# Optimization experiments

Measured on AMD Instinct MI355X. Metric: run time of the kernel, lower is better.

## Reference

```python
import jax, jax.numpy as jnp
import numpy as np

B, NPG, H = 128, 111, 32
N = B * NPG                 # 14208 total nodes
EPG = NPG * (NPG - 1)       # 12210 directed edges per connectome graph
E = B * EPG                 # 1562880 edges total


def setup_inputs() -> dict:
    key = jax.random.key(0)
    # full directed graph (no self loops) within each of the B graphs
    s, d = np.nonzero(~np.eye(NPG, dtype=bool))
    off = (np.arange(B) * NPG)[:, None]
    edge_index = jnp.asarray(
        np.stack([(s[None] + off).ravel(), (d[None] + off).ravel()]),
        dtype=jnp.int32)
    ks = iter(jax.random.split(key, 32))
    def nrm(shape, scale=0.1):
        return (jax.random.normal(next(ks), shape) * scale).astype(jnp.float32)
    inp = {
        'x': nrm((N, 1), 1.0),
        'edge_index': edge_index,
        'edge_attr': nrm((E, 2), 1.0),
    }
    dims = [1, H, H]  # input dim of each GATConv layer
    for l in range(3):
        inp[f'W{l}'] = nrm((dims[l], H))   # lin weight (no bias in PyG lin)
        inp[f'as{l}'] = nrm((H,))          # att_src
        inp[f'ad{l}'] = nrm((H,))          # att_dst
        inp[f'We{l}'] = nrm((2, H))        # lin_edge weight
        inp[f'ae{l}'] = nrm((H,))          # att_edge
        inp[f'b{l}'] = jnp.zeros((H,), jnp.float32)
    inp['lin_W'] = nrm((H, 1))
    inp['lin_b'] = jnp.zeros((1,), jnp.float32)
    return inp


def _gat(x, src, dst, ea, W, a_s, a_d, We, a_e, b):
    """PyG GATConv, heads=1: edge-feature attention + segment softmax over dst."""
    h = x @ W                                                     # [N,H]
    alpha = (h @ a_s)[src] + (h @ a_d)[dst] + (ea @ We) @ a_e     # [E']
    alpha = jax.nn.leaky_relu(alpha, 0.2)
    m = jax.lax.stop_gradient(jax.ops.segment_max(alpha, dst, num_segments=N))
    ex = jnp.exp(alpha - m[dst])
    coef = ex / jax.ops.segment_sum(ex, dst, num_segments=N)[dst]
    return jax.ops.segment_sum(coef[:, None] * h[src], dst, num_segments=N) + b


def reference(x, edge_index, edge_attr,
              W0, as0, ad0, We0, ae0, b0,
              W1, as1, ad1, We1, ae1, b1,
              W2, as2, ad2, We2, ae2, b2,
              lin_W, lin_b):
    src0, dst0 = edge_index[0], edge_index[1]
    # add_self_loops with fill_value='mean': per-dst mean of incoming edge_attr
    deg = jax.ops.segment_sum(jnp.ones((E,), edge_attr.dtype), dst0, num_segments=N)
    ea_loop = jax.ops.segment_sum(edge_attr, dst0, num_segments=N) / jnp.maximum(deg, 1.0)[:, None]
    loop = jnp.arange(N, dtype=src0.dtype)
    src = jnp.concatenate([src0, loop])
    dst = jnp.concatenate([dst0, loop])
    ea = jnp.concatenate([edge_attr, ea_loop], axis=0)

    h = _gat(x, src, dst, ea, W0, as0, ad0, We0, ae0, b0)
    h = _gat(h, src, dst, ea, W1, as1, ad1, We1, ae1, b1)
    h = jax.nn.relu(h)  # Dropout(0.5) is identity in eval
    h = _gat(h, src, dst, ea, W2, as2, ad2, We2, ae2, b2)

    graph_id = jnp.arange(N) // NPG                                # global_add_pool
    pooled = jax.ops.segment_sum(h, graph_id, num_segments=B)      # [B,H]
    return jax.nn.relu(pooled @ lin_W + lin_b)                     # [B,1]
```

## Files before the change

### kernel.cpp

```cpp
#include <hip/hip_runtime.h>
#include <hip/hip_bf16.h>

#define BGR  128
#define NPG  111
#define EPG  (NPG*(NPG-1))
#define H16S 136
#define HRS  40

typedef _Float16 half8 __attribute__((ext_vector_type(8)));
typedef float    f32x4 __attribute__((ext_vector_type(4)));

__global__ __launch_bounds__(1024, 1) void
gnn_all(const float* __restrict__ x, const float* __restrict__ ea,
        const float* __restrict__ W0, const float* __restrict__ as0, const float* __restrict__ ad0,
        const float* __restrict__ We0, const float* __restrict__ ae0, const float* __restrict__ b0,
        const float* __restrict__ W1, const float* __restrict__ as1, const float* __restrict__ ad1,
        const float* __restrict__ We1, const float* __restrict__ ae1, const float* __restrict__ b1,
        const float* __restrict__ W2, const float* __restrict__ as2, const float* __restrict__ ad2,
        const float* __restrict__ We2, const float* __restrict__ ae2, const float* __restrict__ b2,
        const float* __restrict__ linW, const float* __restrict__ linb,
        float* __restrict__ out)
{
    int g = blockIdx.x;
    int t = threadIdx.x;
    int wave = t >> 6, lane = t & 63;
    int m = lane & 15, quad = lane >> 4;

    __shared__ float    eaL[EPG * 2];
    __shared__ _Float16 h16[32 * H16S];
    __shared__ _Float16 hrow[112 * HRS];
    __shared__ float assP[2][112];
    __shared__ float adsP[2][112];
    __shared__ float xsh[112];
    __shared__ float bsh[32];
    __shared__ float pool7[8];

    {
        const float4* eg4 = (const float4*)(ea + (size_t)g * EPG * 2);
        float4* dst = (float4*)eaL;
        for (int i = t; i < EPG / 2; i += 1024) dst[i] = eg4[i];
    }
    if (t < 112) xsh[t] = (t < NPG) ? x[g * NPG + t] : 0.f;
    for (int i = t; i < 32 * H16S; i += 1024) h16[i] = (_Float16)0.f;
    if (t < HRS) hrow[111 * HRS + t] = (_Float16)0.f;

    float kr = (lane < 32) ? W0[lane] * as0[lane] : W0[lane & 31] * ad0[lane & 31];
    #pragma unroll
    for (int off = 1; off < 32; off <<= 1) kr += __shfl_xor(kr, off);
    float K_as = __shfl(kr, 0), K_ad = __shfl(kr, 32);
    __syncthreads();

    for (int l = 0; l < 3; l++) {
        const float* W  = (l == 0) ? W0  : ((l == 1) ? W1  : W2);
        const float* aS = (l == 0) ? as0 : ((l == 1) ? as1 : as2);
        const float* aD = (l == 0) ? ad0 : ((l == 1) ? ad1 : ad2);
        const float* Ne = (l == 0) ? We0 : ((l == 1) ? We1 : We2);
        const float* av = (l == 0) ? ae0 : ((l == 1) ? ae1 : ae2);
        const float* bb = (l == 0) ? b0  : ((l == 1) ? b1  : b2);

        float red = Ne[(lane >> 5) * 32 + (lane & 31)] * av[lane & 31];
        #pragma unroll
        for (int off = 1; off < 32; off <<= 1) red += __shfl_xor(red, off);
        float c0 = __shfl(red, 0), c1 = __shfl(red, 32);

        if (t < 32) bsh[t] = bb[t];

        if (wave < 14) {
            if (l == 0) {
                int c = t & 31, sbase = t >> 5;
                float wc = W[c];
                #pragma unroll
                for (int it = 0; it < 4; it++) {
                    int s = sbase + it * 28;
                    float hv = (s < NPG) ? xsh[s] * wc : 0.f;
                    h16[c * H16S + s] = (_Float16)hv;
                }
                if (t < 112) {
                    assP[0][t] = xsh[t] * K_as;  adsP[0][t] = xsh[t] * K_ad;
                    assP[1][t] = 0.f;            adsP[1][t] = 0.f;
                }
            } else {
                int ct = wave & 1, st = wave >> 1;
                int cb = ct * 16 + m;
                half8 A, B;
                #pragma unroll
                for (int j = 0; j < 8; j++) A[j] = (_Float16)W[(quad * 8 + j) * 32 + cb];
                B = *(const half8*)&hrow[(st * 16 + m) * HRS + quad * 8];
                if (l == 2) {
                    #pragma unroll
                    for (int j = 0; j < 8; j++)
                        B[j] = (B[j] > (_Float16)0.f) ? B[j] : (_Float16)0.f;
                }
                f32x4 D = {0.f, 0.f, 0.f, 0.f};
                D = __builtin_amdgcn_mfma_f32_16x16x32_f16(A, B, D, 0, 0, 0);
                float pa = 0.f, pd = 0.f;
                #pragma unroll
                for (int r = 0; r < 4; r++) {
                    int cc = ct * 16 + quad * 4 + r;
                    h16[cc * H16S + st * 16 + m] = (_Float16)D[r];
                    pa += D[r] * aS[cc];
                    pd += D[r] * aD[cc];
                }
                pa += __shfl_xor(pa, 16); pa += __shfl_xor(pa, 32);
                pd += __shfl_xor(pd, 16); pd += __shfl_xor(pd, 32);
                if (lane < 16) { assP[ct][st * 16 + m] = pa; adsP[ct][st * 16 + m] = pd; }
            }
        }
        __syncthreads();

        if (wave < 7) {
            int d = wave * 16 + m;
            bool dok = (d < NPG);
            float adsv = dok ? (adsP[0][d] + adsP[1][d]) : 0.f;

            float dsum = 0.f;
            if (dok) {
                #pragma unroll 4
                for (int k = 0; k < 28; k++) {
                    int s = quad * 28 + k;
                    if (s < NPG && s != d) {
                        float2 e = *(const float2*)&eaL[2 * (s * 110 + d - (d > s ? 1 : 0))];
                        dsum += c0 * e.x + c1 * e.y;
                    }
                }
            }
            dsum += __shfl_xor(dsum, 16);
            dsum += __shfl_xor(dsum, 32);
            float dval = dsum * (1.f / 110.f);

            f32x4 acc0 = {0.f, 0.f, 0.f, 0.f};
            f32x4 acc1 = {0.f, 0.f, 0.f, 0.f};
            float den = 0.f;
            #pragma unroll
            for (int kc = 0; kc < 4; kc++) {
                int s0 = kc * 32 + quad * 8;
                float4 p0 = *(const float4*)&assP[0][s0];
                float4 p1 = *(const float4*)&assP[1][s0];
                float4 q0 = *(const float4*)&assP[0][s0 + 4];
                float4 q1 = *(const float4*)&assP[1][s0 + 4];
                float asv[8] = {p0.x + p1.x, p0.y + p1.y, p0.z + p1.z, p0.w + p1.w,
                                q0.x + q1.x, q0.y + q1.y, q0.z + q1.z, q0.w + q1.w};
                half8 A;
                #pragma unroll
                for (int j = 0; j < 8; j++) {
                    int s = s0 + j;
                    float p = 0.f;
                    if (dok && s < NPG) {
                        float ev;
                        if (s == d) {
                            ev = dval;
                        } else {
                            float2 e = *(const float2*)&eaL[2 * (s * 110 + d - (d > s ? 1 : 0))];
                            ev = c0 * e.x + c1 * e.y;
                        }
                        float a = asv[j] + adsv + ev;
                        a = (a > 0.f) ? a : 0.2f * a;
                        p = __expf(a);
                    }
                    _Float16 ph = (_Float16)p;
                    A[j] = ph;
                    den += (float)ph;
                }
                half8 B0 = *(const half8*)&h16[(size_t)m * H16S + s0];
                half8 B1 = *(const half8*)&h16[(size_t)(16 + m) * H16S + s0];
                acc0 = __builtin_amdgcn_mfma_f32_16x16x32_f16(A, B0, acc0, 0, 0, 0);
                acc1 = __builtin_amdgcn_mfma_f32_16x16x32_f16(A, B1, acc1, 0, 0, 0);
            }
            den += __shfl_xor(den, 16);
            den += __shfl_xor(den, 32);

            if (l < 2) {
                #pragma unroll
                for (int r = 0; r < 4; r++) {
                    int dr = wave * 16 + quad * 4 + r;
                    float dn = __shfl(den, quad * 4 + r);
                    if (dr < NPG) {
                        float inv = 1.f / dn;
                        hrow[dr * HRS + m]      = (_Float16)(acc0[r] * inv + bsh[m]);
                        hrow[dr * HRS + 16 + m] = (_Float16)(acc1[r] * inv + bsh[16 + m]);
                    }
                }
            } else {
                float lw0 = linW[m], lw1 = linW[16 + m];
                float p = 0.f;
                #pragma unroll
                for (int r = 0; r < 4; r++) {
                    int dr = wave * 16 + quad * 4 + r;
                    float dn = __shfl(den, quad * 4 + r);
                    if (dr < NPG) {
                        float inv = 1.f / dn;
                        p += (acc0[r] * inv + bsh[m]) * lw0
                           + (acc1[r] * inv + bsh[16 + m]) * lw1;
                    }
                }
                #pragma unroll
                for (int off = 1; off < 64; off <<= 1) p += __shfl_xor(p, off);
                if (lane == 0) pool7[wave] = p;
            }
        }
        __syncthreads();
    }

    if (t == 0) {
        float s = 0.f;
        #pragma unroll
        for (int w = 0; w < 7; w++) s += pool7[w];
        out[g] = fmaxf(s + linb[0], 0.f);
    }
}

extern "C" void kernel_launch(void* const* d_in, const int* in_sizes, int n_in,
                              void* d_out, int out_size, void* d_ws, size_t ws_size,
                              hipStream_t stream) {
    const float* x  = (const float*)d_in[0];
    const float* ea = (const float*)d_in[2];
    gnn_all<<<BGR, 1024, 0, stream>>>(
        x, ea,
        (const float*)d_in[3],  (const float*)d_in[4],  (const float*)d_in[5],
        (const float*)d_in[6],  (const float*)d_in[7],  (const float*)d_in[8],
        (const float*)d_in[9],  (const float*)d_in[10], (const float*)d_in[11],
        (const float*)d_in[12], (const float*)d_in[13], (const float*)d_in[14],
        (const float*)d_in[15], (const float*)d_in[16], (const float*)d_in[17],
        (const float*)d_in[18], (const float*)d_in[19], (const float*)d_in[20],
        (const float*)d_in[21], (const float*)d_in[22],
        (float*)d_out);
}
```

Baseline: 138.2 us.

## Halve block size, precompute edge-attr column sums once, preload per-layer params to LDS

The block shrinks from 1024 to 512 threads, and the projection tiles become a loop over waves. The per-destination sum of edge attributes is now computed once in layer 0 and stored in LDS, so layers 1 and 2 no longer rescan the edge attributes. W1/W2 (as fp16), the attention vectors, the biases and the edge coefficients are loaded into LDS up front, and only the h16 padding columns are zeroed. This removes repeated LDS scans and global loads, but fewer waves per block means less latency hiding and some loops now run more iterations per thread.

```diff
diff --git a/kernel.cpp b/kernel.cpp
--- a/kernel.cpp
+++ b/kernel.cpp
@@ -10,7 +10,7 @@
 typedef _Float16 half8 __attribute__((ext_vector_type(8)));
 typedef float    f32x4 __attribute__((ext_vector_type(4)));
 
-__global__ __launch_bounds__(1024, 1) void
+__global__ __launch_bounds__(512, 1) void
 gnn_all(const float* __restrict__ x, const float* __restrict__ ea,
         const float* __restrict__ W0, const float* __restrict__ as0, const float* __restrict__ ad0,
         const float* __restrict__ We0, const float* __restrict__ ae0, const float* __restrict__ b0,
@@ -29,62 +29,99 @@
     __shared__ float    eaL[EPG * 2];
     __shared__ _Float16 h16[32 * H16S];
     __shared__ _Float16 hrow[112 * HRS];
-    __shared__ float assP[2][112];
-    __shared__ float adsP[2][112];
-    __shared__ float xsh[112];
-    __shared__ float bsh[32];
-    __shared__ float pool7[8];
+    __shared__ _Float16 WL[2][1024];
+    __shared__ float    assP[2][128];
+    __shared__ float    adsP[2][128];
+    __shared__ float    colsum2[112][2];
+    __shared__ float    cvL[3][2];
+    __shared__ float    aswL[3][32], adwL[3][32], bshL[3][32];
+    __shared__ float    xsh[112];
+    __shared__ float    pool7[8];
 
     {
         const float4* eg4 = (const float4*)(ea + (size_t)g * EPG * 2);
         float4* dst = (float4*)eaL;
-        for (int i = t; i < EPG / 2; i += 1024) dst[i] = eg4[i];
+        for (int i = t; i < EPG / 2; i += 512) dst[i] = eg4[i];
     }
     if (t < 112) xsh[t] = (t < NPG) ? x[g * NPG + t] : 0.f;
-    for (int i = t; i < 32 * H16S; i += 1024) h16[i] = (_Float16)0.f;
+    for (int i = t; i < 32 * 25; i += 512) {
+        int c = i / 25, s = 111 + (i - c * 25);
+        h16[c * H16S + s] = (_Float16)0.f;
+    }
     if (t < HRS) hrow[111 * HRS + t] = (_Float16)0.f;
-
-    float kr = (lane < 32) ? W0[lane] * as0[lane] : W0[lane & 31] * ad0[lane & 31];
-    #pragma unroll
-    for (int off = 1; off < 32; off <<= 1) kr += __shfl_xor(kr, off);
-    float K_as = __shfl(kr, 0), K_ad = __shfl(kr, 32);
-    __syncthreads();
-
-    for (int l = 0; l < 3; l++) {
-        const float* W  = (l == 0) ? W0  : ((l == 1) ? W1  : W2);
-        const float* aS = (l == 0) ? as0 : ((l == 1) ? as1 : as2);
-        const float* aD = (l == 0) ? ad0 : ((l == 1) ? ad1 : ad2);
+    for (int i = t; i < 1024; i += 512) {
+        WL[0][i] = (_Float16)W1[i];
+        WL[1][i] = (_Float16)W2[i];
+    }
+    if (t < 96) {
+        int l = t >> 5, c = t & 31;
+        const float* aSp = (l == 0) ? as0 : ((l == 1) ? as1 : as2);
+        const float* aDp = (l == 0) ? ad0 : ((l == 1) ? ad1 : ad2);
+        const float* bbp = (l == 0) ? b0  : ((l == 1) ? b1  : b2);
+        aswL[l][c] = aSp[c]; adwL[l][c] = aDp[c]; bshL[l][c] = bbp[c];
+    }
+    if (t < 192) {
+        int l = t >> 6;
         const float* Ne = (l == 0) ? We0 : ((l == 1) ? We1 : We2);
         const float* av = (l == 0) ? ae0 : ((l == 1) ? ae1 : ae2);
-        const float* bb = (l == 0) ? b0  : ((l == 1) ? b1  : b2);
-
         float red = Ne[(lane >> 5) * 32 + (lane & 31)] * av[lane & 31];
         #pragma unroll
         for (int off = 1; off < 32; off <<= 1) red += __shfl_xor(red, off);
-        float c0 = __shfl(red, 0), c1 = __shfl(red, 32);
-
-        if (t < 32) bsh[t] = bb[t];
-
-        if (wave < 14) {
-            if (l == 0) {
-                int c = t & 31, sbase = t >> 5;
-                float wc = W[c];
-                #pragma unroll
-                for (int it = 0; it < 4; it++) {
-                    int s = sbase + it * 28;
-                    float hv = (s < NPG) ? xsh[s] * wc : 0.f;
-                    h16[c * H16S + s] = (_Float16)hv;
-                }
-                if (t < 112) {
-                    assP[0][t] = xsh[t] * K_as;  adsP[0][t] = xsh[t] * K_ad;
-                    assP[1][t] = 0.f;            adsP[1][t] = 0.f;
-                }
-            } else {
-                int ct = wave & 1, st = wave >> 1;
+        if (lane == 0)  cvL[l][0] = red;
+        if (lane == 32) cvL[l][1] = red;
+    }
+    float K_as = 0.f, K_ad = 0.f;
+    if (wave < 2) {
+        float kr = (lane < 32) ? W0[lane] * as0[lane]
+                               : W0[lane & 31] * ad0[lane & 31];
+        #pragma unroll
+        for (int off = 1; off < 32; off <<= 1) kr += __shfl_xor(kr, off);
+        K_as = __shfl(kr, 0); K_ad = __shfl(kr, 32);
+    }
+    __syncthreads();
+
+    for (int l = 0; l < 3; l++) {
+        float2 cv = *(const float2*)&cvL[l][0];
+        float c0 = cv.x, c1 = cv.y;
+
+        if (l == 0) {
+            int c = t & 31, sb = t >> 5;
+            float wc = W0[c];
+            #pragma unroll
+            for (int it = 0; it < 7; it++) {
+                int s = sb + it * 16;
+                float hv = (s < NPG) ? xsh[s] * wc : 0.f;
+                h16[c * H16S + s] = (_Float16)hv;
+            }
+            if (t < 112) {
+                assP[0][t] = xsh[t] * K_as;  adsP[0][t] = xsh[t] * K_ad;
+                assP[1][t] = 0.f;            adsP[1][t] = 0.f;
+            }
+            if (wave < 7) {
+                int d = wave * 16 + m;
+                bool dok = (d < NPG);
+                float sx = 0.f, sy = 0.f;
+                if (dok) {
+                    #pragma unroll 4
+                    for (int k = 0; k < 28; k++) {
+                        int s = quad * 28 + k;
+                        if (s < NPG && s != d) {
+                            float2 e = *(const float2*)&eaL[2 * (s * 110 + d - (d > s ? 1 : 0))];
+                            sx += e.x; sy += e.y;
+                        }
+                    }
+                }
+                sx += __shfl_xor(sx, 16); sx += __shfl_xor(sx, 32);
+                sy += __shfl_xor(sy, 16); sy += __shfl_xor(sy, 32);
+                if (lane < 16 && dok) { colsum2[d][0] = sx; colsum2[d][1] = sy; }
+            }
+        } else {
+            for (int tile = wave; tile < 14; tile += 8) {
+                int ct = tile & 1, st = tile >> 1;
                 int cb = ct * 16 + m;
                 half8 A, B;
                 #pragma unroll
-                for (int j = 0; j < 8; j++) A[j] = (_Float16)W[(quad * 8 + j) * 32 + cb];
+                for (int j = 0; j < 8; j++) A[j] = WL[l - 1][(quad * 8 + j) * 32 + cb];
                 B = *(const half8*)&hrow[(st * 16 + m) * HRS + quad * 8];
                 if (l == 2) {
                     #pragma unroll
@@ -98,8 +135,8 @@
                 for (int r = 0; r < 4; r++) {
                     int cc = ct * 16 + quad * 4 + r;
                     h16[cc * H16S + st * 16 + m] = (_Float16)D[r];
-                    pa += D[r] * aS[cc];
-                    pd += D[r] * aD[cc];
+                    pa += D[r] * aswL[l][cc];
+                    pd += D[r] * adwL[l][cc];
                 }
                 pa += __shfl_xor(pa, 16); pa += __shfl_xor(pa, 32);
                 pd += __shfl_xor(pd, 16); pd += __shfl_xor(pd, 32);
@@ -112,21 +149,11 @@
             int d = wave * 16 + m;
             bool dok = (d < NPG);
             float adsv = dok ? (adsP[0][d] + adsP[1][d]) : 0.f;
-
-            float dsum = 0.f;
+            float dval = 0.f;
             if (dok) {
-                #pragma unroll 4
-                for (int k = 0; k < 28; k++) {
-                    int s = quad * 28 + k;
-                    if (s < NPG && s != d) {
-                        float2 e = *(const float2*)&eaL[2 * (s * 110 + d - (d > s ? 1 : 0))];
-                        dsum += c0 * e.x + c1 * e.y;
-                    }
-                }
-            }
-            dsum += __shfl_xor(dsum, 16);
-            dsum += __shfl_xor(dsum, 32);
-            float dval = dsum * (1.f / 110.f);
+                float2 cs = *(const float2*)&colsum2[d][0];
+                dval = (c0 * cs.x + c1 * cs.y) * (1.f / 110.f);
+            }
 
             f32x4 acc0 = {0.f, 0.f, 0.f, 0.f};
             f32x4 acc1 = {0.f, 0.f, 0.f, 0.f};
@@ -176,8 +203,8 @@
                     float dn = __shfl(den, quad * 4 + r);
                     if (dr < NPG) {
                         float inv = 1.f / dn;
-                        hrow[dr * HRS + m]      = (_Float16)(acc0[r] * inv + bsh[m]);
-                        hrow[dr * HRS + 16 + m] = (_Float16)(acc1[r] * inv + bsh[16 + m]);
+                        hrow[dr * HRS + m]      = (_Float16)(acc0[r] * inv + bshL[l][m]);
+                        hrow[dr * HRS + 16 + m] = (_Float16)(acc1[r] * inv + bshL[l][16 + m]);
                     }
                 }
             } else {
@@ -189,8 +216,8 @@
                     float dn = __shfl(den, quad * 4 + r);
                     if (dr < NPG) {
                         float inv = 1.f / dn;
-                        p += (acc0[r] * inv + bsh[m]) * lw0
-                           + (acc1[r] * inv + bsh[16 + m]) * lw1;
+                        p += (acc0[r] * inv + bshL[2][m]) * lw0
+                           + (acc1[r] * inv + bshL[2][16 + m]) * lw1;
                     }
                 }
                 #pragma unroll
@@ -214,7 +241,7 @@
                               hipStream_t stream) {
     const float* x  = (const float*)d_in[0];
     const float* ea = (const float*)d_in[2];
-    gnn_all<<<BGR, 1024, 0, stream>>>(
+    gnn_all<<<BGR, 512, 0, stream>>>(
         x, ea,
         (const float*)d_in[3],  (const float*)d_in[4],  (const float*)d_in[5],
         (const float*)d_in[6],  (const float*)d_in[7],  (const float*)d_in[8],
```

Result: faster. 130.5 us (-5.6%).
